# Performance work log

Measured on AMD Instinct MI355X. Metric: run time of the kernel, lower is better.

## Reference

```python
import jax, jax.numpy as jnp
import numpy as np

B, T, C, H = 2, 1024, 1024, 16
N = C // H
D_W, D_A, D_V, D_G = 64, 64, 32, 160
VOCAB = 50257


def setup_inputs() -> dict:
    key = jax.random.key(0)
    ks = iter(jax.random.split(key, 48))
    rn = lambda shape, s=1.0: jax.random.normal(next(ks), shape, dtype=jnp.float32) * s
    inp = {
        'residual': rn((B, T, C)),
        'x': rn((B, T, C)),
        'v_first': rn((B, T, C)),
        'x0': rn((B, T, C)),
        'dx0': rn((B, T, C)),
        'token_ids': jax.random.randint(next(ks), (B, T), 0, VOCAB),
        # token-shift mix coefficients (1,1,C), in [0,1) like the 1-pow(ddd,...) init
        'mr': jax.random.uniform(next(ks), (1, 1, C)),
        'mw': jax.random.uniform(next(ks), (1, 1, C)),
        'mk': jax.random.uniform(next(ks), (1, 1, C)),
        'mv': jax.random.uniform(next(ks), (1, 1, C)),
        'ma': jax.random.uniform(next(ks), (1, 1, C)),
        'mg': jax.random.uniform(next(ks), (1, 1, C)),
        # decay LoRA
        'w0': rn((1, 1, C), 1.0) - 1.0,
        'w1': rn((C, D_W), 0.05),
        'w2': rn((D_W, C), 0.05),
        # in-context-learning-rate LoRA
        'a0': rn((1, 1, C), 0.3),
        'a1': rn((C, D_A), 0.05),
        'a2': rn((D_A, C), 0.05),
        # value-residual LoRA
        'v0': rn((1, 1, C), 0.3) + 0.73,
        'v1': rn((C, D_V), 0.05),
        'v2': rn((D_V, C), 0.05),
        # gate LoRA
        'g1': rn((C, D_G), 0.05),
        'g2': rn((D_G, C), 0.05),
        'k_k': rn((1, 1, C), 0.1) + 0.71,
        'k_a': rn((1, 1, C), 0.1) + 1.02,
        'r_k': rn((H, N), 0.1) - 0.04,
        # projections stored as (in, out); y = x @ W (== torch Linear with W.T)
        'W_r': rn((C, C), C ** -0.5),
        'W_k': rn((C, C), 0.1 * C ** -0.5),
        'W_v': rn((C, C), C ** -0.5),
        'W_o': rn((C, C), C ** -0.5),
        'ln_w': jnp.full((C,), ((1 + 12) / 24) ** 0.7, dtype=jnp.float32),
        'ln_b': jnp.zeros((C,), dtype=jnp.float32),
    }
    return inp


def rwkv7_scan(r, log_w, k, v, a, b):
    # all inputs [B,T,H,N]; recurrence per head on state S [N_v, N_k]:
    #   S_t = S_{t-1} * diag(exp(log_w_t)) + S_{t-1} @ (a_t b_t^T) + v_t k_t^T
    #   o_t = S_t @ r_t
    def step(S, inp):
        r_t, w_t, k_t, v_t, a_t, b_t = inp  # each [B,H,N]
        Sa = jnp.einsum('bhvk,bhk->bhv', S, a_t)
        S = (S * jnp.exp(w_t)[:, :, None, :]
             + Sa[..., None] * b_t[:, :, None, :]
             + v_t[..., None] * k_t[:, :, None, :])
        o = jnp.einsum('bhvk,bhk->bhv', S, r_t)
        return S, o

    to_t = lambda z: jnp.moveaxis(z, 1, 0)  # [T,B,H,N]
    S0 = jnp.zeros((r.shape[0], H, N, N), dtype=r.dtype)
    _, o = jax.lax.scan(step, S0, (to_t(r), to_t(log_w), to_t(k), to_t(v), to_t(a), to_t(b)))
    return jnp.moveaxis(o, 0, 1)  # [B,T,H,N]


def group_norm(x, w, b, eps=0.00064):
    # GroupNorm(H, C): normalize each head's N channels per (B,T) position
    Bx, Tx, Cx = x.shape
    xg = x.reshape(Bx, Tx, H, N)
    mu = xg.mean(-1, keepdims=True)
    var = xg.var(-1, keepdims=True)
    xg = (xg - mu) * jax.lax.rsqrt(var + eps)
    return xg.reshape(Bx, Tx, Cx) * w + b


def reference(residual, x, v_first, x0, dx0, token_ids,
              mr, mw, mk, mv, ma, mg,
              w0, w1, w2, a0, a1, a2, v0, v1, v2, g1, g2,
              k_k, k_a, r_k, W_r, W_k, W_v, W_o, ln_w, ln_b):
    Bx, Tx, Cx = x.shape
    # token shift: x_{t-1} - x_t (zero-pad first step)
    xx = jnp.pad(x, ((0, 0), (1, 0), (0, 0)))[:, :Tx] - x
    xr, xw, xk, xv, xa, xg = (x + xx * m for m in (mr, mw, mk, mv, ma, mg))

    r = xr @ W_r
    log_neglog_w = -jax.nn.softplus(-(w0 + jnp.tanh(xw @ w1) @ w2)) - 0.5
    log_w = -jnp.exp(log_neglog_w)  # in (-e^{-0.5}, 0)
    k = xk @ W_k
    v = xv @ W_v
    v = v + (v_first - v) * jax.nn.sigmoid(v0 + (xv @ v1) @ v2)
    a = jax.nn.sigmoid(a0 + (xa @ a1) @ a2)
    g = jax.nn.sigmoid(xg @ g1) @ g2

    kk = (k * k_k).reshape(Bx, Tx, H, N)
    kk = kk / jnp.maximum(jnp.linalg.norm(kk, axis=-1, keepdims=True), 1e-12)
    k = k * (1 + (a - 1) * k_a)

    r4 = r.reshape(Bx, Tx, H, N)
    w4 = log_w.reshape(Bx, Tx, H, N)
    k4 = k.reshape(Bx, Tx, H, N)
    v4 = v.reshape(Bx, Tx, H, N)
    aa = -kk
    bb = kk * a.reshape(Bx, Tx, H, N)

    o = rwkv7_scan(r4, w4, k4, v4, aa, bb)  # [B,T,H,N]
    y = group_norm(o.reshape(Bx, Tx, Cx), ln_w, ln_b)
    y = y + ((r4 * k4 * r_k).sum(-1, keepdims=True) * v4).reshape(Bx, Tx, Cx)
    y = (y * g) @ W_o
    return residual + y
```

## Files before the change

kernel.cpp:

```cpp
#include <hip/hip_runtime.h>
#include <math.h>

#define B_DIM 2
#define T_SEQ 1024
#define C_DIM 1024
#define H_DIM 16
#define N_DIM 64
#define M_ROWS (B_DIM * T_SEQ)

#define GBM 64
#define GBN 64
#define GBK 64
#define LDK 88

#define SW(r, c) ((c) ^ (((((r) >> 3) & 3)) << 3))

typedef __attribute__((ext_vector_type(8))) short bf16x8;
typedef __attribute__((ext_vector_type(4))) float f32x4;
typedef unsigned short ushortx4 __attribute__((ext_vector_type(4)));
typedef unsigned short ushortx8 __attribute__((ext_vector_type(8)));

__device__ __forceinline__ unsigned short f2bf(float f) {
    unsigned int u = __float_as_uint(f);
    u = (u + 0x7FFFu + ((u >> 16) & 1u)) >> 16;
    return (unsigned short)u;
}
__device__ __forceinline__ float bf2f(unsigned short h) {
    return __uint_as_float(((unsigned int)h) << 16);
}

__device__ __forceinline__ float wred64(float v) {
#pragma unroll
    for (int m = 32; m; m >>= 1) v += __shfl_xor(v, m);
    return v;
}

__global__ __launch_bounds__(256) void premix_kernel(
    const float* __restrict__ x,
    const float* mr, const float* mk, const float* mv,
    const float* mw, const float* ma, const float* mg,
    unsigned short* xr, unsigned short* xk, unsigned short* xv,
    unsigned short* xw, unsigned short* xa, unsigned short* xg)
{
    const int g = blockIdx.x * 256 + threadIdx.x;
    const size_t base = (size_t)g * 8;
    const int row = (int)(base >> 10);
    const int col = (int)(base & 1023);
    const int t_in = row & (T_SEQ - 1);

    const float* xp = x + (size_t)row * C_DIM + col;
    float4 a0 = *(const float4*)xp;
    float4 a1 = *(const float4*)(xp + 4);
    float4 p0 = make_float4(0.f, 0.f, 0.f, 0.f), p1 = p0;
    if (t_in > 0) {
        p0 = *(const float4*)(xp - C_DIM);
        p1 = *(const float4*)(xp - C_DIM + 4);
    }
    const float d0x = p0.x - a0.x, d0y = p0.y - a0.y, d0z = p0.z - a0.z, d0w = p0.w - a0.w;
    const float d1x = p1.x - a1.x, d1y = p1.y - a1.y, d1z = p1.z - a1.z, d1w = p1.w - a1.w;

    const float* ms[6] = {mr, mk, mv, mw, ma, mg};
    unsigned short* outs[6] = {xr, xk, xv, xw, xa, xg};
#pragma unroll
    for (int i = 0; i < 6; ++i) {
        const float4 m0 = *(const float4*)(ms[i] + col);
        const float4 m1 = *(const float4*)(ms[i] + col + 4);
        ushortx8 o;
        o[0] = f2bf(fmaf(d0x, m0.x, a0.x));
        o[1] = f2bf(fmaf(d0y, m0.y, a0.y));
        o[2] = f2bf(fmaf(d0z, m0.z, a0.z));
        o[3] = f2bf(fmaf(d0w, m0.w, a0.w));
        o[4] = f2bf(fmaf(d1x, m1.x, a1.x));
        o[5] = f2bf(fmaf(d1y, m1.y, a1.y));
        o[6] = f2bf(fmaf(d1z, m1.z, a1.z));
        o[7] = f2bf(fmaf(d1w, m1.w, a1.w));
        *(ushortx8*)(outs[i] + base) = o;
    }
}

__global__ __launch_bounds__(256) void wtrans_kernel(
    const float* __restrict__ W, unsigned short* __restrict__ WT)
{
    __shared__ float tile[32][33];
    const int tx = threadIdx.x, ty = threadIdx.y;
    const int n0 = blockIdx.x * 32, k0 = blockIdx.y * 32;
#pragma unroll
    for (int i = 0; i < 4; ++i)
        tile[ty + i * 8][tx] = W[(size_t)(k0 + ty + i * 8) * 1024 + n0 + tx];
    __syncthreads();
#pragma unroll
    for (int i = 0; i < 4; ++i)
        WT[(size_t)(n0 + ty + i * 8) * 1024 + k0 + tx] = f2bf(tile[tx][ty + i * 8]);
}

__global__ __launch_bounds__(256) void trans_all_kernel(
    const float* Wk, const float* Wv, const float* Wr,
    const float* w1p, const float* a1p, const float* v1p, const float* g1p,
    const float* a2p, const float* v2p, const float* g2p, const float* w2p,
    unsigned short* wtA, unsigned short* wtB, unsigned short* wtC,
    unsigned short* wt_w1, unsigned short* wt_a1, unsigned short* wt_v1,
    unsigned short* wt_g1, unsigned short* wt_a2, unsigned short* wt_v2,
    unsigned short* wt_g2, unsigned short* wt_w2)
{
    __shared__ float tile[32][33];
    const int bid = blockIdx.x;
    const float* W; unsigned short* WT; int K, N, t0;
    if      (bid < 1024) { W = Wk;  WT = wtA;   K = 1024; N = 1024; t0 = 0;    }
    else if (bid < 2048) { W = Wv;  WT = wtB;   K = 1024; N = 1024; t0 = 1024; }
    else if (bid < 3072) { W = Wr;  WT = wtC;   K = 1024; N = 1024; t0 = 2048; }
    else if (bid < 3136) { W = w1p; WT = wt_w1; K = 1024; N = 64;   t0 = 3072; }
    else if (bid < 3200) { W = a1p; WT = wt_a1; K = 1024; N = 64;   t0 = 3136; }
    else if (bid < 3232) { W = v1p; WT = wt_v1; K = 1024; N = 32;   t0 = 3200; }
    else if (bid < 3392) { W = g1p; WT = wt_g1; K = 1024; N = 160;  t0 = 3232; }
    else if (bid < 3456) { W = a2p; WT = wt_a2; K = 64;   N = 1024; t0 = 3392; }
    else if (bid < 3488) { W = v2p; WT = wt_v2; K = 32;   N = 1024; t0 = 3456; }
    else if (bid < 3648) { W = g2p; WT = wt_g2; K = 160;  N = 1024; t0 = 3488; }
    else                 { W = w2p; WT = wt_w2; K = 64;   N = 1024; t0 = 3648; }
    const int lt = bid - t0;
    const int ntx = N >> 5;
    const int n0 = (lt % ntx) * 32;
    const int k0 = (lt / ntx) * 32;
    const int tx = threadIdx.x, ty = threadIdx.y;
#pragma unroll
    for (int i = 0; i < 4; ++i)
        tile[ty + i * 8][tx] = W[(size_t)(k0 + ty + i * 8) * N + n0 + tx];
    __syncthreads();
#pragma unroll
    for (int i = 0; i < 4; ++i)
        WT[(size_t)(n0 + ty + i * 8) * K + k0 + tx] = f2bf(tile[tx][ty + i * 8]);
}

__device__ __forceinline__ void gemm_core(
    const unsigned short* __restrict__ Aarr, int arow_stride,
    const unsigned short* __restrict__ WT, int K, int Nc, int bn0, int bm0,
    unsigned short* outp, int ostr, int ooff,
    unsigned short* outh, int hoff, int post)
{
    __shared__ unsigned short As[GBM][LDK];
    __shared__ unsigned short Bs[GBN][LDK];

    const int tid = threadIdx.x;
    const int lane = tid & 63;
    const int wid = tid >> 6;
    const int wr = wid >> 1, wc = wid & 1;
    const int l15 = lane & 15, l4 = lane >> 4;

    const int ar = tid >> 2;
    const int as = (tid & 3) << 4;
    const int row = bm0 + ar;
    const int brn = tid >> 2;
    const int bks = (tid & 3) << 4;
    const bool bn_ok = (bn0 + brn) < Nc;

    const int ra0 = wr * 32 + l15, ra1 = wr * 32 + 16 + l15;
    const int rb0 = wc * 32 + l15, rb1 = wc * 32 + 16 + l15;

    f32x4 acc[2][2] = {};

    for (int k0 = 0; k0 < K; k0 += GBK) {
#pragma unroll
        for (int i = 0; i < 2; ++i) {
            const int kk = as + 8 * i;
            ushortx8 av = {0, 0, 0, 0, 0, 0, 0, 0};
            if (k0 + kk < K)
                av = *(const ushortx8*)(Aarr + (size_t)row * arow_stride + k0 + kk);
            *(ushortx8*)&As[ar][SW(ar, kk)] = av;
        }
#pragma unroll
        for (int i = 0; i < 2; ++i) {
            const int kk = bks + 8 * i;
            ushortx8 bv = {0, 0, 0, 0, 0, 0, 0, 0};
            if (bn_ok && (k0 + kk < K))
                bv = *(const ushortx8*)(WT + (size_t)(bn0 + brn) * K + k0 + kk);
            *(ushortx8*)&Bs[brn][SW(brn, kk)] = bv;
        }
        __syncthreads();
#pragma unroll
        for (int ks = 0; ks < 2; ++ks) {
            const int cc = ks * 32 + l4 * 8;
            bf16x8 af0 = *(const bf16x8*)&As[ra0][SW(ra0, cc)];
            bf16x8 af1 = *(const bf16x8*)&As[ra1][SW(ra1, cc)];
            bf16x8 bg0 = *(const bf16x8*)&Bs[rb0][SW(rb0, cc)];
            bf16x8 bg1 = *(const bf16x8*)&Bs[rb1][SW(rb1, cc)];
            acc[0][0] = __builtin_amdgcn_mfma_f32_16x16x32_bf16(af0, bg0, acc[0][0], 0, 0, 0);
            acc[0][1] = __builtin_amdgcn_mfma_f32_16x16x32_bf16(af0, bg1, acc[0][1], 0, 0, 0);
            acc[1][0] = __builtin_amdgcn_mfma_f32_16x16x32_bf16(af1, bg0, acc[1][0], 0, 0, 0);
            acc[1][1] = __builtin_amdgcn_mfma_f32_16x16x32_bf16(af1, bg1, acc[1][1], 0, 0, 0);
        }
        __syncthreads();
    }

#pragma unroll
    for (int fi = 0; fi < 2; ++fi)
#pragma unroll
        for (int fj = 0; fj < 2; ++fj) {
            const int ocol = bn0 + wc * 32 + fj * 16 + l15;
            if (ocol < Nc) {
#pragma unroll
                for (int p = 0; p < 4; ++p) {
                    const int orow = bm0 + wr * 32 + fi * 16 + l4 * 4 + p;
                    float v = acc[fi][fj][p];
                    if (post == 1) v = tanhf(v);
                    else if (post == 2) v = 1.0f / (1.0f + expf(-v));
                    if (outh)
                        outh[(size_t)orow * 320 + hoff + ocol] = f2bf(v);
                    else
                        outp[((size_t)orow * 1024 + ocol) * ostr + ooff] = f2bf(v);
                }
            }
        }
}

__global__ __launch_bounds__(256) void gemm_s1_kernel(
    const unsigned short* xr, const unsigned short* xk, const unsigned short* xv,
    const unsigned short* xw, const unsigned short* xa, const unsigned short* xg,
    const unsigned short* wtA, const unsigned short* wtB, const unsigned short* wtC,
    const unsigned short* wt_a1, const unsigned short* wt_v1,
    const unsigned short* wt_g1, const unsigned short* wt_w1,
    unsigned short* b_r, unsigned short* pk_bf, unsigned short* b_v,
    unsigned short* h_cat)
{
    const int nt = blockIdx.x;
    const int bm0 = blockIdx.y * GBM;
    const unsigned short* A; const unsigned short* WT;
    unsigned short* outp = nullptr; unsigned short* outh = nullptr;
    int Nc = 1024, nb = 0, ostr = 1, ooff = 0, hoff = 0, post = 0;
    if (nt < 16)      { A = xr; WT = wtC; outp = b_r; nb = nt; }
    else if (nt < 32) { A = xk; WT = wtA; outp = pk_bf; ostr = 4; ooff = 1; nb = nt - 16; }
    else if (nt < 48) { A = xv; WT = wtB; outp = b_v; nb = nt - 32; }
    else if (nt == 48){ A = xa; WT = wt_a1; outh = h_cat; hoff = 0;   Nc = 64; }
    else if (nt == 49){ A = xv; WT = wt_v1; outh = h_cat; hoff = 64;  Nc = 32; }
    else if (nt < 53) { A = xg; WT = wt_g1; outh = h_cat; hoff = 96;  Nc = 160; nb = nt - 50; post = 2; }
    else              { A = xw; WT = wt_w1; outh = h_cat; hoff = 256; Nc = 64; post = 1; }
    gemm_core(A, 1024, WT, 1024, Nc, nb * 64, bm0, outp, ostr, ooff, outh, hoff, post);
}

__global__ __launch_bounds__(256) void gemm_s2_kernel(
    const unsigned short* __restrict__ h_cat,
    const unsigned short* wt_a2, const unsigned short* wt_v2,
    const unsigned short* wt_g2, const unsigned short* wt_w2,
    unsigned short* pk_bf, unsigned short* b_g)
{
    const int g = blockIdx.x >> 4;
    const int nb = blockIdx.x & 15;
    const int bm0 = blockIdx.y * GBM;
    const unsigned short* WT;
    unsigned short* outp; int K, aoff, ostr, ooff;
    if      (g == 0) { WT = wt_a2; K = 64;  aoff = 0;   outp = pk_bf; ostr = 4; ooff = 2; }
    else if (g == 1) { WT = wt_v2; K = 32;  aoff = 64;  outp = pk_bf; ostr = 4; ooff = 3; }
    else if (g == 2) { WT = wt_g2; K = 160; aoff = 96;  outp = b_g;   ostr = 1; ooff = 0; }
    else             { WT = wt_w2; K = 64;  aoff = 256; outp = pk_bf; ostr = 4; ooff = 0; }
    gemm_core(h_cat + aoff, 320, WT, K, 1024, nb * 64, bm0, outp, ostr, ooff, nullptr, 0, 0);
}

__global__ __launch_bounds__(256) void gemm_final_kernel(
    const unsigned short* __restrict__ Y, const unsigned short* __restrict__ WT,
    const float* __restrict__ addend, float* __restrict__ out)
{
    const int K = 1024;
    __shared__ unsigned short As[GBM][LDK];
    __shared__ unsigned short Bs[GBN][LDK];

    const int tid = threadIdx.x;
    const int lane = tid & 63;
    const int wid = tid >> 6;
    const int wr = wid >> 1, wc = wid & 1;
    const int l15 = lane & 15, l4 = lane >> 4;
    const int bm0 = blockIdx.y * GBM;
    const int bn0 = blockIdx.x * GBN;
    const int ar = tid >> 2;
    const int as = (tid & 3) << 4;
    const int row = bm0 + ar;
    const int brn = tid >> 2;
    const int bks = (tid & 3) << 4;

    const int ra0 = wr * 32 + l15, ra1 = wr * 32 + 16 + l15;
    const int rb0 = wc * 32 + l15, rb1 = wc * 32 + 16 + l15;

    f32x4 acc[2][2] = {};

    for (int k0 = 0; k0 < K; k0 += GBK) {
#pragma unroll
        for (int i = 0; i < 2; ++i) {
            const int kk = as + 8 * i;
            *(ushortx8*)&As[ar][SW(ar, kk)] =
                *(const ushortx8*)(Y + (size_t)row * 1024 + k0 + kk);
        }
#pragma unroll
        for (int i = 0; i < 2; ++i) {
            const int kk = bks + 8 * i;
            *(ushortx8*)&Bs[brn][SW(brn, kk)] =
                *(const ushortx8*)(WT + (size_t)(bn0 + brn) * K + k0 + kk);
        }
        __syncthreads();
#pragma unroll
        for (int ks = 0; ks < 2; ++ks) {
            const int cc = ks * 32 + l4 * 8;
            bf16x8 af0 = *(const bf16x8*)&As[ra0][SW(ra0, cc)];
            bf16x8 af1 = *(const bf16x8*)&As[ra1][SW(ra1, cc)];
            bf16x8 bg0 = *(const bf16x8*)&Bs[rb0][SW(rb0, cc)];
            bf16x8 bg1 = *(const bf16x8*)&Bs[rb1][SW(rb1, cc)];
            acc[0][0] = __builtin_amdgcn_mfma_f32_16x16x32_bf16(af0, bg0, acc[0][0], 0, 0, 0);
            acc[0][1] = __builtin_amdgcn_mfma_f32_16x16x32_bf16(af0, bg1, acc[0][1], 0, 0, 0);
            acc[1][0] = __builtin_amdgcn_mfma_f32_16x16x32_bf16(af1, bg0, acc[1][0], 0, 0, 0);
            acc[1][1] = __builtin_amdgcn_mfma_f32_16x16x32_bf16(af1, bg1, acc[1][1], 0, 0, 0);
        }
        __syncthreads();
    }

#pragma unroll
    for (int fi = 0; fi < 2; ++fi)
#pragma unroll
        for (int fj = 0; fj < 2; ++fj) {
            const int ocol = bn0 + wc * 32 + fj * 16 + l15;
#pragma unroll
            for (int p = 0; p < 4; ++p) {
                const int orow = bm0 + wr * 32 + fi * 16 + l4 * 4 + p;
                out[(size_t)orow * 1024 + ocol] =
                    acc[fi][fj][p] + addend[(size_t)orow * 1024 + ocol];
            }
        }
}

__global__ __launch_bounds__(256) void chunk_prep_kernel(
    const unsigned short* __restrict__ pk_bf,
    const unsigned short* __restrict__ b_r,
    unsigned short* __restrict__ b_v,
    const float* __restrict__ v_first,
    const float* w0, const float* a0, const float* v0,
    const float* k_k, const float* k_a, const float* r_k,
    float* __restrict__ TB,
    unsigned short* __restrict__ Gt, unsigned short* __restrict__ LRt,
    float* __restrict__ Vc, float* __restrict__ Wl,
    unsigned short* __restrict__ Oi)
{
    __shared__ __align__(16) char smem[60800];
    unsigned short (*tB)[72]  = (unsigned short (*)[72])(smem + 0);
    unsigned short (*tK)[72]  = (unsigned short (*)[72])(smem + 4608);
    unsigned short (*tR)[72]  = (unsigned short (*)[72])(smem + 9216);
    unsigned short (*tBT)[40] = (unsigned short (*)[40])(smem + 13824);
    unsigned short (*VlT)[40] = (unsigned short (*)[40])(smem + 18944);
    unsigned short (*egT)[40] = (unsigned short (*)[40])(smem + 24064);
    float (*W32s)[66]         = (float (*)[66])(smem + 26624);
    float (*fg)[33]           = (float (*)[33])(smem + 35072);
    unsigned short (*tA)[72]  = (unsigned short (*)[72])(smem + 39296);
    float (*cg)[33]           = (float (*)[33])(smem + 43904);
    unsigned short (*ZB)[40]  = (unsigned short (*)[40])(smem + 39296);
    unsigned short (*DhB)[40] = (unsigned short (*)[40])(smem + 44416);
    float (*dg)[33]           = (float (*)[33])(smem + 48128);
    unsigned short (*fT)[40]  = (unsigned short (*)[40])(smem + 48128);
    float* EWZ                = (float*)(smem + 52352);
    unsigned short (*KtT)[40] = (unsigned short (*)[40])(smem + 52352);

    const int tid = threadIdx.x;
    const int lane = tid & 63;
    const int w = tid >> 6;
    const int l15 = lane & 15, l4 = lane >> 4;
    const int bhc = blockIdx.x;
    const int bh = bhc >> 5, ck = bhc & 31;
    const int b = bh >> 4, h = bh & 15;
    const int cglob = h * 64 + lane;

    const float kkc = k_k[cglob], kac = k_a[cglob];
    const float a0c = a0[cglob], v0c = v0[cglob];
    const float w0c = w0[cglob], rkc = r_k[cglob];
#pragma unroll
    for (int q = 0; q < 8; ++q) {
        const int tq = w * 8 + q;
        const int row = b * 1024 + ck * 32 + tq;
        const size_t gi = (size_t)row * 1024 + cglob;
        const ushortx4 pk = *(const ushortx4*)(pk_bf + gi * 4);
        const float kl = bf2f(pk.y);
        const float kkv = kl * kkc;
        const float ss = wred64(kkv * kkv);
        const float kkn = kkv / fmaxf(sqrtf(ss), 1e-12f);
        const float a = 1.0f / (1.0f + expf(-(a0c + bf2f(pk.z))));
        const float u = w0c + bf2f(pk.x);
        const float ew = expf(-expf(-log1pf(expf(-u)) - 0.5f));
        const float sv = 1.0f / (1.0f + expf(-(v0c + bf2f(pk.w))));
        const float vl = bf2f(b_v[gi]);
        const float v = fmaf(v_first[gi] - vl, sv, vl);
        const float ko = kl * (1.0f + (a - 1.0f) * kac);
        const unsigned short rbf = b_r[gi];
        const float r1f = bf2f(rbf);
        const unsigned short vbf = f2bf(v);
        b_v[gi] = vbf;

        const float t3 = wred64(r1f * ko * rkc);
        if (lane == 0) TB[bh * 1024 + ck * 32 + tq] = t3;

        EWZ[tq * 64 + lane] = ew;
        tA[tq][lane] = f2bf(-kkn);
        tB[tq][lane] = f2bf(kkn * a);
        tK[tq][lane] = f2bf(ko);
        tR[tq][lane] = rbf;
        VlT[lane][tq] = vbf;
    }
    __syncthreads();

    if (w == 0) {
        float run = 1.0f;
        for (int t = 0; t < 32; ++t) {
            run *= EWZ[t * 64 + lane];
            W32s[t][lane] = run;
        }
    }
    __syncthreads();

#pragma unroll
    for (int q = 0; q < 8; ++q) {
        const int tq = w * 8 + q;
        const float Wt = W32s[tq][lane];
        const float Wm1 = tq ? W32s[tq - 1][lane] : 1.0f;
        const float iw = 1.0f / Wt;
        tA[tq][lane] = f2bf(bf2f(tA[tq][lane]) * Wm1);
        const unsigned short tb = f2bf(bf2f(tB[tq][lane]) * iw);
        tB[tq][lane] = tb;
        tBT[lane][tq] = tb;
        tK[tq][lane] = f2bf(bf2f(tK[tq][lane]) * iw);
        tR[tq][lane] = f2bf(bf2f(tR[tq][lane]) * Wt);
    }
    __syncthreads();

    {
        const unsigned short (*Am)[72] = (w == 0 || w == 2) ? tB : tK;
        const unsigned short (*Bm)[72] = (w < 2) ? tA : tR;
        f32x4 gacc[2][2] = {};
#pragma unroll
        for (int kh = 0; kh < 2; ++kh) {
            const int cc = kh * 32 + l4 * 8;
            bf16x8 ax0 = *(const bf16x8*)&Am[l15][cc];
            bf16x8 ax1 = *(const bf16x8*)&Am[16 + l15][cc];
            bf16x8 bx0 = *(const bf16x8*)&Bm[l15][cc];
            bf16x8 bx1 = *(const bf16x8*)&Bm[16 + l15][cc];
            gacc[0][0] = __builtin_amdgcn_mfma_f32_16x16x32_bf16(ax0, bx0, gacc[0][0], 0, 0, 0);
            gacc[0][1] = __builtin_amdgcn_mfma_f32_16x16x32_bf16(ax0, bx1, gacc[0][1], 0, 0, 0);
            gacc[1][0] = __builtin_amdgcn_mfma_f32_16x16x32_bf16(ax1, bx0, gacc[1][0], 0, 0, 0);
            gacc[1][1] = __builtin_amdgcn_mfma_f32_16x16x32_bf16(ax1, bx1, gacc[1][1], 0, 0, 0);
        }
#pragma unroll
        for (int mt = 0; mt < 2; ++mt)
#pragma unroll
            for (int nt = 0; nt < 2; ++nt) {
                const int col = nt * 16 + l15;
                if (w == 2) {
                    ushortx4 st;
#pragma unroll
                    for (int p = 0; p < 4; ++p) st[p] = f2bf(gacc[mt][nt][p]);
                    *(ushortx4*)&egT[col][mt * 16 + l4 * 4] = st;
                } else {
#pragma unroll
                    for (int p = 0; p < 4; ++p) {
                        const int rw = mt * 16 + l4 * 4 + p;
                        if (w == 0) cg[rw][col] = gacc[mt][nt][p];
                        else if (w == 1) dg[rw][col] = gacc[mt][nt][p];
                        else fg[rw][col] = gacc[mt][nt][p];
                    }
                }
            }
    }
    __syncthreads();

#pragma unroll
    for (int p = 0; p < 4; ++p) {
        const int idx = tid * 4 + p;
        const int r_ = idx >> 5, c_ = idx & 31;
        if (r_ >= c_) cg[r_][c_] = 0.0f;
        if (c_ <= r_) dg[r_][c_] = 0.0f;
        if (r_ > c_) fg[r_][c_] = 0.0f;
        if (c_ > r_) egT[r_][c_] = 0;
    }
    __syncthreads();

    if (w == 0) {
        for (int i = 0; i < 32; ++i) {
            float val = bf2f(tA[i][lane]);
            for (int j = 0; j < i; ++j) val += cg[j][i] * EWZ[lane * 33 + j];
            EWZ[lane * 33 + i] = val;
        }
    } else if (w == 1 && lane < 32) {
        for (int t = 0; t < 32; ++t) {
            float val = dg[lane][t];
            for (int j = 0; j < t; ++j) val += cg[j][t] * dg[lane][j];
            dg[lane][t] = val;
        }
    }
    __syncthreads();

#pragma unroll
    for (int p = 0; p < 4; ++p) {
        const int idx = tid * 4 + p;
        DhB[idx >> 5][idx & 31] = f2bf(dg[idx >> 5][idx & 31]);
    }
#pragma unroll
    for (int p = 0; p < 8; ++p) {
        const int idx = tid * 8 + p;
        ZB[idx >> 5][idx & 31] = f2bf(EWZ[(idx >> 5) * 33 + (idx & 31)]);
    }
    __syncthreads();

    const size_t cb2048 = (size_t)bhc * 2048;
    const size_t cb4096 = (size_t)bhc * 4096;

    if (w == 0) {
#pragma unroll
        for (int mt = 0; mt < 2; ++mt)
#pragma unroll
            for (int nt = 0; nt < 2; ++nt) {
                f32x4 cacc;
#pragma unroll
                for (int p = 0; p < 4; ++p) cacc[p] = fg[mt * 16 + l4 * 4 + p][nt * 16 + l15];
                bf16x8 ax = *(const bf16x8*)&DhB[mt * 16 + l15][l4 * 8];
                bf16x8 bx = *(const bf16x8*)&egT[nt * 16 + l15][l4 * 8];
                cacc = __builtin_amdgcn_mfma_f32_16x16x32_bf16(ax, bx, cacc, 0, 0, 0);
                ushortx4 st;
#pragma unroll
                for (int p = 0; p < 4; ++p) st[p] = f2bf(cacc[p]);
                *(ushortx4*)&fT[nt * 16 + l15][mt * 16 + l4 * 4] = st;
            }
    } else if (w == 1) {
#pragma unroll
        for (int mt = 0; mt < 2; ++mt)
#pragma unroll
            for (int nt = 0; nt < 4; ++nt) {
                bf16x8 ax = *(const bf16x8*)&DhB[mt * 16 + l15][l4 * 8];
                bf16x8 bx = *(const bf16x8*)&tBT[nt * 16 + l15][l4 * 8];
                f32x4 cacc = {};
                cacc = __builtin_amdgcn_mfma_f32_16x16x32_bf16(ax, bx, cacc, 0, 0, 0);
                const int col = nt * 16 + l15;
                const float w31c = W32s[31][col];
                ushortx4 st;
#pragma unroll
                for (int p = 0; p < 4; ++p) {
                    const int rw = mt * 16 + l4 * 4 + p;
                    st[p] = f2bf((cacc[p] + bf2f(tK[rw][col])) * w31c);
                }
                *(ushortx4*)&KtT[col][mt * 16 + l4 * 4] = st;
            }
    } else if (w == 2) {
#pragma unroll
        for (int mt = 0; mt < 4; ++mt)
#pragma unroll
            for (int nt = 0; nt < 4; ++nt) {
                bf16x8 ax = *(const bf16x8*)&tBT[mt * 16 + l15][l4 * 8];
                bf16x8 bx = *(const bf16x8*)&ZB[nt * 16 + l15][l4 * 8];
                f32x4 cacc = {};
                cacc = __builtin_amdgcn_mfma_f32_16x16x32_bf16(ax, bx, cacc, 0, 0, 0);
                const int kcol = nt * 16 + l15;
#pragma unroll
                for (int p = 0; p < 4; ++p) {
                    const int n_ = mt * 16 + l4 * 4 + p;
                    LRt[cb4096 + n_ * 64 + kcol] = f2bf(cacc[p] * W32s[31][n_]);
                }
            }
    } else {
#pragma unroll
        for (int mt = 0; mt < 2; ++mt)
#pragma unroll
            for (int nt = 0; nt < 4; ++nt) {
                bf16x8 ax = *(const bf16x8*)&egT[mt * 16 + l15][l4 * 8];
                bf16x8 bx = *(const bf16x8*)&ZB[nt * 16 + l15][l4 * 8];
                f32x4 cacc = {};
                cacc = __builtin_amdgcn_mfma_f32_16x16x32_bf16(ax, bx, cacc, 0, 0, 0);
                const int ncol = nt * 16 + l15;
#pragma unroll
                for (int p = 0; p < 4; ++p) {
                    const int t_ = mt * 16 + l4 * 4 + p;
                    Gt[cb2048 + t_ * 64 + ncol] = f2bf(cacc[p] + bf2f(tR[t_][ncol]));
                }
            }
    }
    __syncthreads();

    if (w < 2) {
#pragma unroll
        for (int mt = 0; mt < 2; ++mt)
#pragma unroll
            for (int ntl = 0; ntl < 2; ++ntl) {
                const int nt = w * 2 + ntl;
                bf16x8 ax = *(const bf16x8*)&fT[mt * 16 + l15][l4 * 8];
                bf16x8 bx = *(const bf16x8*)&VlT[nt * 16 + l15][l4 * 8];
                f32x4 cacc = {};
                cacc = __builtin_amdgcn_mfma_f32_16x16x32_bf16(ax, bx, cacc, 0, 0, 0);
                const int vcol = nt * 16 + l15;
#pragma unroll
                for (int p = 0; p < 4; ++p) {
                    const int t_ = mt * 16 + l4 * 4 + p;
                    Oi[cb2048 + t_ * 64 + vcol] = f2bf(cacc[p]);
                }
            }
    } else {
#pragma unroll
        for (int mtl = 0; mtl < 2; ++mtl)
#pragma unroll
            for (int nt = 0; nt < 4; ++nt) {
                const int mt = (w - 2) * 2 + mtl;
                bf16x8 ax = *(const bf16x8*)&VlT[mt * 16 + l15][l4 * 8];
                bf16x8 bx = *(const bf16x8*)&KtT[nt * 16 + l15][l4 * 8];
                f32x4 cacc = {};
                cacc = __builtin_amdgcn_mfma_f32_16x16x32_bf16(ax, bx, cacc, 0, 0, 0);
                const int ncol = nt * 16 + l15;
                float4 st = make_float4(cacc[0], cacc[1], cacc[2], cacc[3]);
                *(float4*)&Vc[cb4096 + (size_t)ncol * 64 + mt * 16 + l4 * 4] = st;
            }
    }
    if (tid < 64) Wl[(size_t)bhc * 64 + tid] = W32s[31][tid];
}

struct SeqRegs {
    bf16x8 g[4];
    bf16x8 lr[8];
    float4 vc[4];
    float wl[4];
    ushortx4 oi[2];
};

__device__ __forceinline__ void load_chunk(
    SeqRegs& R,
    const unsigned short* __restrict__ gt, const unsigned short* __restrict__ lr,
    const float* __restrict__ vct, const float* __restrict__ wlp,
    const unsigned short* __restrict__ oi, int l15, int l4, int vg)
{
#pragma unroll
    for (int tt = 0; tt < 2; ++tt) {
        R.g[tt * 2 + 0] = *(const bf16x8*)&gt[(tt * 16 + l15) * 64 + l4 * 8];
        R.g[tt * 2 + 1] = *(const bf16x8*)&gt[(tt * 16 + l15) * 64 + 32 + l4 * 8];
        R.oi[tt] = *(const ushortx4*)&oi[(tt * 16 + l15) * 64 + vg * 16 + l4 * 4];
    }
#pragma unroll
    for (int nt = 0; nt < 4; ++nt) {
        R.lr[nt * 2 + 0] = *(const bf16x8*)&lr[(nt * 16 + l15) * 64 + l4 * 8];
        R.lr[nt * 2 + 1] = *(const bf16x8*)&lr[(nt * 16 + l15) * 64 + 32 + l4 * 8];
        R.vc[nt] = *(const float4*)&vct[(nt * 16 + l15) * 64 + vg * 16 + l4 * 4];
        R.wl[nt] = wlp[nt * 16 + l15];
    }
}

__device__ __forceinline__ void seq_step(
    f32x4* sC, const SeqRegs& R, unsigned short (*Sst)[80],
    unsigned short* __restrict__ o, int b, int h, int c, int vg, int l15, int l4)
{
#pragma unroll
    for (int nt = 0; nt < 4; ++nt)
#pragma unroll
        for (int p = 0; p < 4; ++p)
            Sst[l4 * 4 + p][nt * 16 + l15] = f2bf(sC[nt][p]);
    __builtin_amdgcn_wave_barrier();
    bf16x8 a0 = *(const bf16x8*)&Sst[l15][l4 * 8];
    bf16x8 a1 = *(const bf16x8*)&Sst[l15][32 + l4 * 8];
    __builtin_amdgcn_wave_barrier();

    f32x4 oacc[2] = {};
#pragma unroll
    for (int tt = 0; tt < 2; ++tt) {
        oacc[tt] = __builtin_amdgcn_mfma_f32_16x16x32_bf16(a0, R.g[tt * 2 + 0], oacc[tt], 0, 0, 0);
        oacc[tt] = __builtin_amdgcn_mfma_f32_16x16x32_bf16(a1, R.g[tt * 2 + 1], oacc[tt], 0, 0, 0);
    }
    f32x4 lac[4] = {};
#pragma unroll
    for (int nt = 0; nt < 4; ++nt) {
        lac[nt] = __builtin_amdgcn_mfma_f32_16x16x32_bf16(a0, R.lr[nt * 2 + 0], lac[nt], 0, 0, 0);
        lac[nt] = __builtin_amdgcn_mfma_f32_16x16x32_bf16(a1, R.lr[nt * 2 + 1], lac[nt], 0, 0, 0);
    }

#pragma unroll
    for (int nt = 0; nt < 4; ++nt) {
        const float wlv = R.wl[nt];
#pragma unroll
        for (int p = 0; p < 4; ++p)
            sC[nt][p] = sC[nt][p] * wlv + lac[nt][p] + R.vc[nt][p];
    }

#pragma unroll
    for (int tt = 0; tt < 2; ++tt) {
        const int trow = b * 1024 + c * 32 + tt * 16 + l15;
        ushortx4 ov;
        ov.x = f2bf(oacc[tt][0] + bf2f(R.oi[tt].x));
        ov.y = f2bf(oacc[tt][1] + bf2f(R.oi[tt].y));
        ov.z = f2bf(oacc[tt][2] + bf2f(R.oi[tt].z));
        ov.w = f2bf(oacc[tt][3] + bf2f(R.oi[tt].w));
        *(ushortx4*)(o + (size_t)trow * 1024 + h * 64 + vg * 16 + l4 * 4) = ov;
    }
}

__global__ __launch_bounds__(64) void chunk_seq_kernel(
    const unsigned short* __restrict__ Gt, const unsigned short* __restrict__ LRt,
    const float* __restrict__ VcT, const float* __restrict__ Wl,
    const unsigned short* __restrict__ Oi, unsigned short* __restrict__ o)
{
    __shared__ unsigned short Sst[16][80];
    const int lane = threadIdx.x & 63;
    const int bid = blockIdx.x;
    const int bh = bid >> 2, vg = bid & 3;
    const int b = bh >> 4, h = bh & 15;
    const int l15 = lane & 15, l4 = lane >> 4;

    const size_t cbase = (size_t)bh * 32;
    const unsigned short* gt = Gt + cbase * 2048;
    const unsigned short* lr = LRt + cbase * 4096;
    const float* vct = VcT + cbase * 4096;
    const float* wlp = Wl + cbase * 64;
    const unsigned short* oi = Oi + cbase * 2048;

    f32x4 sC[4] = {};
    SeqRegs RA, RB;
    load_chunk(RA, gt, lr, vct, wlp, oi, l15, l4, vg);

    for (int cc = 0; cc < 16; ++cc) {
        const int c0 = cc * 2, c1 = cc * 2 + 1;
        load_chunk(RB, gt + (size_t)c1 * 2048, lr + (size_t)c1 * 4096,
                   vct + (size_t)c1 * 4096, wlp + (size_t)c1 * 64,
                   oi + (size_t)c1 * 2048, l15, l4, vg);
        seq_step(sC, RA, Sst, o, b, h, c0, vg, l15, l4);
        const int c2 = (c1 + 1 < 32) ? c1 + 1 : 31;
        load_chunk(RA, gt + (size_t)c2 * 2048, lr + (size_t)c2 * 4096,
                   vct + (size_t)c2 * 4096, wlp + (size_t)c2 * 64,
                   oi + (size_t)c2 * 2048, l15, l4, vg);
        seq_step(sC, RB, Sst, o, b, h, c1, vg, l15, l4);
    }
}

__global__ __launch_bounds__(256) void post_kernel(
    const unsigned short* o, const unsigned short* v, const unsigned short* g,
    const float* __restrict__ TB,
    const float* ln_w, const float* ln_b,
    unsigned short* y)
{
    const int gw = (blockIdx.x * blockDim.x + threadIdx.x) >> 6;
    const int lane = threadIdx.x & 63;
    const int row = gw >> 4;
    const int h = gw & 15;
    const int c = h * N_DIM + lane;
    const size_t idx = (size_t)row * C_DIM + c;
    const int b = row >> 10;
    const int t = row & 1023;

    const float oo = bf2f(o[idx]);
    float s1 = oo, s2 = oo * oo;
#pragma unroll
    for (int m = 32; m; m >>= 1) {
        s1 += __shfl_xor(s1, m);
        s2 += __shfl_xor(s2, m);
    }
    const float mu = s1 * (1.0f / 64.0f);
    const float var = s2 * (1.0f / 64.0f) - mu * mu;
    float yv = (oo - mu) * rsqrtf(var + 0.00064f);
    yv = yv * ln_w[c] + ln_b[c];

    yv += TB[(b * 16 + h) * 1024 + t] * bf2f(v[idx]);
    y[idx] = f2bf(yv * bf2f(g[idx]));
}

extern "C" void kernel_launch(void* const* d_in, const int* in_sizes, int n_in,
                              void* d_out, int out_size, void* d_ws, size_t ws_size,
                              hipStream_t stream) {
    (void)in_sizes; (void)n_in; (void)out_size; (void)ws_size;

    const float* residual = (const float*)d_in[0];
    const float* x        = (const float*)d_in[1];
    const float* v_first  = (const float*)d_in[2];
    const float* mr = (const float*)d_in[6];
    const float* mw = (const float*)d_in[7];
    const float* mk = (const float*)d_in[8];
    const float* mv = (const float*)d_in[9];
    const float* ma = (const float*)d_in[10];
    const float* mg = (const float*)d_in[11];
    const float* w0 = (const float*)d_in[12];
    const float* w1 = (const float*)d_in[13];
    const float* w2 = (const float*)d_in[14];
    const float* a0 = (const float*)d_in[15];
    const float* a1 = (const float*)d_in[16];
    const float* a2 = (const float*)d_in[17];
    const float* v0 = (const float*)d_in[18];
    const float* v1 = (const float*)d_in[19];
    const float* v2 = (const float*)d_in[20];
    const float* g1 = (const float*)d_in[21];
    const float* g2 = (const float*)d_in[22];
    const float* k_k = (const float*)d_in[23];
    const float* k_a = (const float*)d_in[24];
    const float* r_k = (const float*)d_in[25];
    const float* W_r = (const float*)d_in[26];
    const float* W_k = (const float*)d_in[27];
    const float* W_v = (const float*)d_in[28];
    const float* W_o = (const float*)d_in[29];
    const float* ln_w = (const float*)d_in[30];
    const float* ln_b = (const float*)d_in[31];

    float* out = (float*)d_out;
    char* wsb = (char*)d_ws;

    unsigned short* xr = (unsigned short*)(wsb + 0);
    unsigned short* xk = (unsigned short*)(wsb + 4194304);
    unsigned short* xv = (unsigned short*)(wsb + 8388608);
    unsigned short* xw = (unsigned short*)(wsb + 12582912);
    unsigned short* xa = (unsigned short*)(wsb + 16777216);
    unsigned short* xg = (unsigned short*)(wsb + 20971520);
    float* Vc          = (float*)(wsb + 0);
    unsigned short* Gt = (unsigned short*)(wsb + 16777216);
    unsigned short* Oi = (unsigned short*)(wsb + 20971520);
    unsigned short* pk_bf = (unsigned short*)(wsb + 25165824);
    unsigned short* wtD = (unsigned short*)(wsb + 25165824);
    unsigned short* y_bf = (unsigned short*)(wsb + 27262976);
    unsigned short* b_r = (unsigned short*)(wsb + 41943040);
    unsigned short* b_v = (unsigned short*)(wsb + 46137344);
    unsigned short* b_o = (unsigned short*)(wsb + 50331648);
    unsigned short* b_g = (unsigned short*)(wsb + 54525952);
    unsigned short* h_cat = (unsigned short*)(wsb + 58720256);
    unsigned short* wt_a1 = (unsigned short*)(wsb + 60293120);
    unsigned short* wt_v1 = (unsigned short*)(wsb + 60424192);
    unsigned short* wt_g1 = (unsigned short*)(wsb + 60489728);
    unsigned short* wt_a2 = (unsigned short*)(wsb + 60817408);
    unsigned short* wt_v2 = (unsigned short*)(wsb + 60948480);
    unsigned short* wt_g2 = (unsigned short*)(wsb + 61014016);
    unsigned short* wt_w1 = (unsigned short*)(wsb + 61341696);
    unsigned short* wt_w2 = (unsigned short*)(wsb + 61472768);
    unsigned short* wtA = (unsigned short*)(wsb + 61603840);
    unsigned short* wtB = (unsigned short*)(wsb + 63700992);
    unsigned short* wtC = (unsigned short*)(wsb + 65798144);
    unsigned short* LRt = (unsigned short*)(wsb + 60030976);
    float* Wl = (float*)(wsb + 68419584);
    float* TB = (float*)(wsb + 68681728);

    const dim3 blk(256);
    const dim3 tblk(32, 8);

    premix_kernel<<<dim3(1024), blk, 0, stream>>>(
        x, mr, mk, mv, mw, ma, mg, xr, xk, xv, xw, xa, xg);

    trans_all_kernel<<<dim3(3712), tblk, 0, stream>>>(
        W_k, W_v, W_r, w1, a1, v1, g1, a2, v2, g2, w2,
        wtA, wtB, wtC, wt_w1, wt_a1, wt_v1, wt_g1, wt_a2, wt_v2, wt_g2, wt_w2);

    gemm_s1_kernel<<<dim3(54, 32), blk, 0, stream>>>(
        xr, xk, xv, xw, xa, xg, wtA, wtB, wtC,
        wt_a1, wt_v1, wt_g1, wt_w1, b_r, pk_bf, b_v, h_cat);

    gemm_s2_kernel<<<dim3(64, 32), blk, 0, stream>>>(
        h_cat, wt_a2, wt_v2, wt_g2, wt_w2, pk_bf, b_g);

    chunk_prep_kernel<<<dim3(1024), blk, 0, stream>>>(
        pk_bf, b_r, b_v, v_first, w0, a0, v0, k_k, k_a, r_k,
        TB, Gt, LRt, Vc, Wl, Oi);

    wtrans_kernel<<<dim3(32, 32), tblk, 0, stream>>>(W_o, wtD);

    chunk_seq_kernel<<<dim3(128), dim3(64), 0, stream>>>(Gt, LRt, Vc, Wl, Oi, b_o);

    post_kernel<<<dim3(8192), blk, 0, stream>>>(
        b_o, b_v, b_g, TB, ln_w, ln_b, y_bf);

    gemm_final_kernel<<<dim3(16, 32), blk, 0, stream>>>(y_bf, wtD, residual, out);
}
```

Before: 165.2 us.

## Use 128x128 tiles for the big projection GEMMs and split the small LoRA GEMMs

The three 1024x1024 projection GEMMs (r, k, v) and the final output GEMM now use a new 128x128 tile core with K-step 32 and 4x4 MFMA fragments per wave, which raises arithmetic intensity per shared-memory load. The small LoRA-down GEMMs move to a separate launch that keeps the 64-tile core. The larger tiles cut global and LDS traffic per FLOP, but the grid shrinks (384 blocks for stage 1, 128 for the final GEMM), which may underfill the MI355X CUs. Each K step also has less work to hide its two barriers, and there is one extra kernel launch.

```diff
diff --git a/kernel.cpp b/kernel.cpp
--- a/kernel.cpp
+++ b/kernel.cpp
@@ -12,8 +12,8 @@
 #define GBN 64
 #define GBK 64
 #define LDK 88
-
 #define SW(r, c) ((c) ^ (((((r) >> 3) & 3)) << 3))
+#define SW16(r, c) ((c) ^ ((((r) >> 3) & 1) << 4))
 
 typedef __attribute__((ext_vector_type(8))) short bf16x8;
 typedef __attribute__((ext_vector_type(4))) float f32x4;
@@ -211,28 +211,108 @@
         }
 }
 
-__global__ __launch_bounds__(256) void gemm_s1_kernel(
-    const unsigned short* xr, const unsigned short* xk, const unsigned short* xv,
-    const unsigned short* xw, const unsigned short* xa, const unsigned short* xg,
-    const unsigned short* wtA, const unsigned short* wtB, const unsigned short* wtC,
+__device__ __forceinline__ void gemm128_core(
+    const unsigned short* __restrict__ A,
+    const unsigned short* __restrict__ WT,
+    int bm0, int bn0,
+    unsigned short (*As)[40], unsigned short (*Bs)[40],
+    f32x4 (*acc)[4])
+{
+    const int tid = threadIdx.x;
+    const int lane = tid & 63;
+    const int w = tid >> 6;
+    const int wr = w >> 1, wc = w & 1;
+    const int l15 = lane & 15, l4 = lane >> 4;
+    const int sr = tid >> 1;
+    const int sc = (tid & 1) << 4;
+    const int ssc = SW16(sr, sc);
+
+    const unsigned short* ap = A + (size_t)(bm0 + sr) * 1024 + sc;
+    const unsigned short* bp = WT + (size_t)(bn0 + sr) * 1024 + sc;
+
+    for (int k0 = 0; k0 < 1024; k0 += 32) {
+        ushortx8 av0 = *(const ushortx8*)(ap + k0);
+        ushortx8 av1 = *(const ushortx8*)(ap + k0 + 8);
+        ushortx8 bv0 = *(const ushortx8*)(bp + k0);
+        ushortx8 bv1 = *(const ushortx8*)(bp + k0 + 8);
+        *(ushortx8*)&As[sr][ssc] = av0;
+        *(ushortx8*)&As[sr][ssc + 8] = av1;
+        *(ushortx8*)&Bs[sr][ssc] = bv0;
+        *(ushortx8*)&Bs[sr][ssc + 8] = bv1;
+        __syncthreads();
+        bf16x8 af[4], bg[4];
+#pragma unroll
+        for (int f = 0; f < 4; ++f) {
+            const int ra = wr * 64 + f * 16 + l15;
+            const int rb = wc * 64 + f * 16 + l15;
+            af[f] = *(const bf16x8*)&As[ra][SW16(ra, l4 * 8)];
+            bg[f] = *(const bf16x8*)&Bs[rb][SW16(rb, l4 * 8)];
+        }
+#pragma unroll
+        for (int fi = 0; fi < 4; ++fi)
+#pragma unroll
+            for (int fj = 0; fj < 4; ++fj)
+                acc[fi][fj] = __builtin_amdgcn_mfma_f32_16x16x32_bf16(
+                    af[fi], bg[fj], acc[fi][fj], 0, 0, 0);
+        __syncthreads();
+    }
+}
+
+__global__ __launch_bounds__(256) void gemm_s1big_kernel(
+    const unsigned short* __restrict__ xr, const unsigned short* __restrict__ xk,
+    const unsigned short* __restrict__ xv,
+    const unsigned short* __restrict__ wtC, const unsigned short* __restrict__ wtA,
+    const unsigned short* __restrict__ wtB,
+    unsigned short* __restrict__ b_r, unsigned short* __restrict__ pk_bf,
+    unsigned short* __restrict__ b_v)
+{
+    __shared__ unsigned short As[128][40];
+    __shared__ unsigned short Bs[128][40];
+    const int g = blockIdx.x >> 3;
+    const int bn0 = (blockIdx.x & 7) * 128;
+    const int bm0 = blockIdx.y * 128;
+    const unsigned short* A = (g == 0) ? xr : (g == 1) ? xk : xv;
+    const unsigned short* WT = (g == 0) ? wtC : (g == 1) ? wtA : wtB;
+
+    f32x4 acc[4][4] = {};
+    gemm128_core(A, WT, bm0, bn0, As, Bs, acc);
+
+    const int lane = threadIdx.x & 63;
+    const int w = threadIdx.x >> 6;
+    const int wr = w >> 1, wc = w & 1;
+    const int l15 = lane & 15, l4 = lane >> 4;
+#pragma unroll
+    for (int fi = 0; fi < 4; ++fi)
+#pragma unroll
+        for (int fj = 0; fj < 4; ++fj) {
+            const int ocol = bn0 + wc * 64 + fj * 16 + l15;
+#pragma unroll
+            for (int p = 0; p < 4; ++p) {
+                const int orow = bm0 + wr * 64 + fi * 16 + l4 * 4 + p;
+                const unsigned short hv = f2bf(acc[fi][fj][p]);
+                if (g == 0) b_r[(size_t)orow * 1024 + ocol] = hv;
+                else if (g == 1) pk_bf[((size_t)orow * 1024 + ocol) * 4 + 1] = hv;
+                else b_v[(size_t)orow * 1024 + ocol] = hv;
+            }
+        }
+}
+
+__global__ __launch_bounds__(256) void gemm_s1small_kernel(
+    const unsigned short* xa, const unsigned short* xv, const unsigned short* xg,
+    const unsigned short* xw,
     const unsigned short* wt_a1, const unsigned short* wt_v1,
     const unsigned short* wt_g1, const unsigned short* wt_w1,
-    unsigned short* b_r, unsigned short* pk_bf, unsigned short* b_v,
     unsigned short* h_cat)
 {
     const int nt = blockIdx.x;
     const int bm0 = blockIdx.y * GBM;
     const unsigned short* A; const unsigned short* WT;
-    unsigned short* outp = nullptr; unsigned short* outh = nullptr;
-    int Nc = 1024, nb = 0, ostr = 1, ooff = 0, hoff = 0, post = 0;
-    if (nt < 16)      { A = xr; WT = wtC; outp = b_r; nb = nt; }
-    else if (nt < 32) { A = xk; WT = wtA; outp = pk_bf; ostr = 4; ooff = 1; nb = nt - 16; }
-    else if (nt < 48) { A = xv; WT = wtB; outp = b_v; nb = nt - 32; }
-    else if (nt == 48){ A = xa; WT = wt_a1; outh = h_cat; hoff = 0;   Nc = 64; }
-    else if (nt == 49){ A = xv; WT = wt_v1; outh = h_cat; hoff = 64;  Nc = 32; }
-    else if (nt < 53) { A = xg; WT = wt_g1; outh = h_cat; hoff = 96;  Nc = 160; nb = nt - 50; post = 2; }
-    else              { A = xw; WT = wt_w1; outh = h_cat; hoff = 256; Nc = 64; post = 1; }
-    gemm_core(A, 1024, WT, 1024, Nc, nb * 64, bm0, outp, ostr, ooff, outh, hoff, post);
+    int Nc, nb = 0, hoff, post = 0;
+    if (nt == 0)      { A = xa; WT = wt_a1; hoff = 0;   Nc = 64; }
+    else if (nt == 1) { A = xv; WT = wt_v1; hoff = 64;  Nc = 32; }
+    else if (nt < 5)  { A = xg; WT = wt_g1; hoff = 96;  Nc = 160; nb = nt - 2; post = 2; }
+    else              { A = xw; WT = wt_w1; hoff = 256; Nc = 64; post = 1; }
+    gemm_core(A, 1024, WT, 1024, Nc, nb * 64, bm0, nullptr, 1, 0, h_cat, hoff, post);
 }
 
 __global__ __launch_bounds__(256) void gemm_s2_kernel(
@@ -253,69 +333,30 @@
     gemm_core(h_cat + aoff, 320, WT, K, 1024, nb * 64, bm0, outp, ostr, ooff, nullptr, 0, 0);
 }
 
-__global__ __launch_bounds__(256) void gemm_final_kernel(
+__global__ __launch_bounds__(256) void gemm_final128_kernel(
     const unsigned short* __restrict__ Y, const unsigned short* __restrict__ WT,
     const float* __restrict__ addend, float* __restrict__ out)
 {
-    const int K = 1024;
-    __shared__ unsigned short As[GBM][LDK];
-    __shared__ unsigned short Bs[GBN][LDK];
-
-    const int tid = threadIdx.x;
-    const int lane = tid & 63;
-    const int wid = tid >> 6;
-    const int wr = wid >> 1, wc = wid & 1;
+    __shared__ unsigned short As[128][40];
+    __shared__ unsigned short Bs[128][40];
+    const int bn0 = blockIdx.x * 128;
+    const int bm0 = blockIdx.y * 128;
+
+    f32x4 acc[4][4] = {};
+    gemm128_core(Y, WT, bm0, bn0, As, Bs, acc);
+
+    const int lane = threadIdx.x & 63;
+    const int w = threadIdx.x >> 6;
+    const int wr = w >> 1, wc = w & 1;
     const int l15 = lane & 15, l4 = lane >> 4;
-    const int bm0 = blockIdx.y * GBM;
-    const int bn0 = blockIdx.x * GBN;
-    const int ar = tid >> 2;
-    const int as = (tid & 3) << 4;
-    const int row = bm0 + ar;
-    const int brn = tid >> 2;
-    const int bks = (tid & 3) << 4;
-
-    const int ra0 = wr * 32 + l15, ra1 = wr * 32 + 16 + l15;
-    const int rb0 = wc * 32 + l15, rb1 = wc * 32 + 16 + l15;
-
-    f32x4 acc[2][2] = {};
-
-    for (int k0 = 0; k0 < K; k0 += GBK) {
-#pragma unroll
-        for (int i = 0; i < 2; ++i) {
-            const int kk = as + 8 * i;
-            *(ushortx8*)&As[ar][SW(ar, kk)] =
-                *(const ushortx8*)(Y + (size_t)row * 1024 + k0 + kk);
-        }
-#pragma unroll
-        for (int i = 0; i < 2; ++i) {
-            const int kk = bks + 8 * i;
-            *(ushortx8*)&Bs[brn][SW(brn, kk)] =
-                *(const ushortx8*)(WT + (size_t)(bn0 + brn) * K + k0 + kk);
-        }
-        __syncthreads();
-#pragma unroll
-        for (int ks = 0; ks < 2; ++ks) {
-            const int cc = ks * 32 + l4 * 8;
-            bf16x8 af0 = *(const bf16x8*)&As[ra0][SW(ra0, cc)];
-            bf16x8 af1 = *(const bf16x8*)&As[ra1][SW(ra1, cc)];
-            bf16x8 bg0 = *(const bf16x8*)&Bs[rb0][SW(rb0, cc)];
-            bf16x8 bg1 = *(const bf16x8*)&Bs[rb1][SW(rb1, cc)];
-            acc[0][0] = __builtin_amdgcn_mfma_f32_16x16x32_bf16(af0, bg0, acc[0][0], 0, 0, 0);
-            acc[0][1] = __builtin_amdgcn_mfma_f32_16x16x32_bf16(af0, bg1, acc[0][1], 0, 0, 0);
-            acc[1][0] = __builtin_amdgcn_mfma_f32_16x16x32_bf16(af1, bg0, acc[1][0], 0, 0, 0);
-            acc[1][1] = __builtin_amdgcn_mfma_f32_16x16x32_bf16(af1, bg1, acc[1][1], 0, 0, 0);
-        }
-        __syncthreads();
-    }
-
-#pragma unroll
-    for (int fi = 0; fi < 2; ++fi)
-#pragma unroll
-        for (int fj = 0; fj < 2; ++fj) {
-            const int ocol = bn0 + wc * 32 + fj * 16 + l15;
+#pragma unroll
+    for (int fi = 0; fi < 4; ++fi)
+#pragma unroll
+        for (int fj = 0; fj < 4; ++fj) {
+            const int ocol = bn0 + wc * 64 + fj * 16 + l15;
 #pragma unroll
             for (int p = 0; p < 4; ++p) {
-                const int orow = bm0 + wr * 32 + fi * 16 + l4 * 4 + p;
+                const int orow = bm0 + wr * 64 + fi * 16 + l4 * 4 + p;
                 out[(size_t)orow * 1024 + ocol] =
                     acc[fi][fj][p] + addend[(size_t)orow * 1024 + ocol];
             }
@@ -831,9 +872,11 @@
         W_k, W_v, W_r, w1, a1, v1, g1, a2, v2, g2, w2,
         wtA, wtB, wtC, wt_w1, wt_a1, wt_v1, wt_g1, wt_a2, wt_v2, wt_g2, wt_w2);
 
-    gemm_s1_kernel<<<dim3(54, 32), blk, 0, stream>>>(
-        xr, xk, xv, xw, xa, xg, wtA, wtB, wtC,
-        wt_a1, wt_v1, wt_g1, wt_w1, b_r, pk_bf, b_v, h_cat);
+    gemm_s1big_kernel<<<dim3(24, 16), blk, 0, stream>>>(
+        xr, xk, xv, wtC, wtA, wtB, b_r, pk_bf, b_v);
+
+    gemm_s1small_kernel<<<dim3(6, 32), blk, 0, stream>>>(
+        xa, xv, xg, xw, wt_a1, wt_v1, wt_g1, wt_w1, h_cat);
 
     gemm_s2_kernel<<<dim3(64, 32), blk, 0, stream>>>(
         h_cat, wt_a2, wt_v2, wt_g2, wt_w2, pk_bf, b_g);
@@ -849,5 +892,5 @@
     post_kernel<<<dim3(8192), blk, 0, stream>>>(
         b_o, b_v, b_g, TB, ln_w, ln_b, y_bf);
 
-    gemm_final_kernel<<<dim3(16, 32), blk, 0, stream>>>(y_bf, wtD, residual, out);
-}
+    gemm_final128_kernel<<<dim3(8, 16), blk, 0, stream>>>(y_bf, wtD, residual, out);
+}
```

Result: slower. 192.4 us (+16.5%).
